# Kernel optimization log

Measured on AMD Instinct MI355X. Metric: run time of the kernel, lower is better.

The kernel has to match this reference:

```python
import jax, jax.numpy as jnp
import numpy as np

CLAMP_MIN = 1e-30
DIAG_SCALE = 10.0


def _fast_cdist(x1, x2):
    # mean-center both by x1's row-mean (as in torch source)
    adjustment = x1.mean(axis=-2, keepdims=True)
    x1 = x1 - adjustment
    x2 = x2 - adjustment
    x1_norm = jnp.sum(x1 * x1, axis=-1, keepdims=True)  # [N,1]
    x2_norm = jnp.sum(x2 * x2, axis=-1, keepdims=True)  # [N,1]
    # matmul trick: ||a-b||^2 = ||a||^2 + ||b||^2 - 2 a.b
    res = (-2.0) * (x1 @ x2.T) + x1_norm + x2_norm.T
    return jnp.sqrt(jnp.maximum(res, CLAMP_MIN))


def reference(x):
    # L2-normalize rows
    norm = jnp.linalg.norm(x, axis=-1, keepdims=True)
    x_norm = x / norm
    dist_mat = _fast_cdist(x_norm, x_norm)  # [N, N]
    d = jnp.diagonal(dist_mat)
    dist_mat = dist_mat + DIAG_SCALE * jnp.diag(1.0 - d)
    loss = jnp.max(1.0 / dist_mat, axis=1)
    return jnp.mean(loss)


def setup_inputs() -> dict:
    key = jax.random.key(0)
    x = jax.random.normal(key, (8192, 256), dtype=jnp.float32)
    return {"x": x}
```

## Files before the change

kernel.cpp:

```cpp
#include <hip/hip_runtime.h>
#include <stdint.h>

#define N_ROWS 8192
#define N_DIM  256
#define NB     64
#define NTRI   2080

typedef __attribute__((ext_vector_type(8))) short bf16x8;
typedef __attribute__((ext_vector_type(4))) float f32x4;

__device__ inline unsigned short f2bf(float f) {
    unsigned u = __float_as_uint(f);
    unsigned r = (u + 0x7FFFu + ((u >> 16) & 1u)) >> 16;
    return (unsigned short)r;
}
__device__ inline float bf2f(unsigned short b) {
    return __uint_as_float(((unsigned)b) << 16);
}
__device__ inline unsigned encf(float f) {
    unsigned u = __float_as_uint(f);
    return u ^ ((u & 0x80000000u) ? 0xFFFFFFFFu : 0x80000000u);
}
__device__ inline float decf(unsigned e) {
    unsigned u = e ^ ((e & 0x80000000u) ? 0x80000000u : 0xFFFFFFFFu);
    return __uint_as_float(u);
}
#define ENC_BIG 0xF149F2CAu


__global__ __launch_bounds__(256) void k_norm_fast(const float* __restrict__ x,
                                                   char* __restrict__ zf,
                                                   float* __restrict__ nsq,
                                                   unsigned* __restrict__ rmin,
                                                   float* __restrict__ out) {
    if (blockIdx.x == 0 && threadIdx.x == 0) *out = 0.0f;
    const int lane = threadIdx.x & 63;
    const int w    = threadIdx.x >> 6;
    const int row  = blockIdx.x * 4 + w;
    const float4* xr = (const float4*)(x + (size_t)row * N_DIM);
    float4 v = xr[lane];
    float ss = v.x*v.x + v.y*v.y + v.z*v.z + v.w*v.w;
    #pragma unroll
    for (int m = 1; m < 64; m <<= 1) ss += __shfl_xor(ss, m, 64);
    const float inv = 1.0f / sqrtf(ss);
    unsigned short b0 = f2bf(v.x * inv);
    unsigned short b1 = f2bf(v.y * inv);
    unsigned short b2 = f2bf(v.z * inv);
    unsigned short b3 = f2bf(v.w * inv);
    ushort4 uv; uv.x = b0; uv.y = b1; uv.z = b2; uv.w = b3;
    *(ushort4*)(zf + ((size_t)(row >> 4) << 13) + ((lane >> 1) << 8) +
                ((row & 15) << 4) + ((lane & 1) << 3)) = uv;
    float z0 = bf2f(b0), z1 = bf2f(b1), z2 = bf2f(b2), z3 = bf2f(b3);
    float s2 = z0*z0 + z1*z1 + z2*z2 + z3*z3;
    #pragma unroll
    for (int m = 1; m < 64; m <<= 1) s2 += __shfl_xor(s2, m, 64);
    if (lane == 0) {
        nsq[row]  = s2;
        rmin[row] = ENC_BIG;
    }
}

__global__ __launch_bounds__(256, 3) void k_gemm_fast(const char* __restrict__ zf,
                                                      const float* __restrict__ nsq,
                                                      unsigned* __restrict__ rmin) {
    __shared__ float pminR[128][2];
    __shared__ float pminC[128][2];

    const int tid   = threadIdx.x;
    const int lane  = tid & 63;
    const int w     = tid >> 6;
    const int waveM = (w >> 1) * 64;
    const int waveN = (w & 1) * 64;

    const int t = blockIdx.x;
    int br = (int)((129.0f - sqrtf(16641.0f - 8.0f * (float)t)) * 0.5f);
    while ((br + 1) * (129 - (br + 1)) / 2 <= t) ++br;
    while (br * (129 - br) / 2 > t) --br;
    const int bc = br + (t - br * (129 - br) / 2);
    const bool isdiag = (br == bc);

    const int aBlk = br * 8 + (waveM >> 4);
    const int bBlk = bc * 8 + (waveN >> 4);

    f32x4 acc[4][4];
    #pragma unroll
    for (int m = 0; m < 4; ++m)
        #pragma unroll
        for (int n = 0; n < 4; ++n)
            acc[m][n] = (f32x4){0.f, 0.f, 0.f, 0.f};

    const char* laneA = zf + (size_t)aBlk * 8192 + lane * 16;
    const char* laneB = zf + (size_t)bBlk * 8192 + lane * 16;

    #pragma unroll
    for (int s = 0; s < 8; ++s) {
        bf16x8 af[4], bfr[4];
        #pragma unroll
        for (int m = 0; m < 4; ++m)
            af[m] = *(const bf16x8*)(laneA + (size_t)m * 8192 + s * 1024);
        #pragma unroll
        for (int n = 0; n < 4; ++n)
            bfr[n] = *(const bf16x8*)(laneB + (size_t)n * 8192 + s * 1024);
        #pragma unroll
        for (int m = 0; m < 4; ++m)
            #pragma unroll
            for (int n = 0; n < 4; ++n)
                acc[m][n] = __builtin_amdgcn_mfma_f32_16x16x32_bf16(af[m], bfr[n], acc[m][n], 0, 0, 0);
    }

    asm volatile("" ::: "memory");

    float nj[4];
    #pragma unroll
    for (int n = 0; n < 4; ++n)
        nj[n] = nsq[bc * 128 + waveN + n * 16 + (lane & 15)];
    float4 ni4[4];
    #pragma unroll
    for (int m = 0; m < 4; ++m)
        ni4[m] = *(const float4*)&nsq[br * 128 + waveM + m * 16 + (lane >> 4) * 4];

    float rminv[4][4];
    float cminv[4];
    #pragma unroll
    for (int m = 0; m < 4; ++m)
        #pragma unroll
        for (int r = 0; r < 4; ++r)
            rminv[m][r] = 1e30f;
    #pragma unroll
    for (int n = 0; n < 4; ++n)
        cminv[n] = 1e30f;

    const int lrow0 = waveM + (lane >> 4) * 4;
    const int lcol0 = waveN + (lane & 15);
    #pragma unroll
    for (int m = 0; m < 4; ++m) {
        #pragma unroll
        for (int r = 0; r < 4; ++r) {
            const int lr = lrow0 + m * 16 + r;
            const float nir = ((const float*)&ni4[m])[r];
            #pragma unroll
            for (int n = 0; n < 4; ++n) {
                float u = fmaf(-2.0f, acc[m][n][r], nir + nj[n]);
                const bool diag = isdiag && (lr == (lcol0 + n * 16));
                u = diag ? 1e30f : u;
                rminv[m][r] = fminf(rminv[m][r], u);
                cminv[n]    = fminf(cminv[n], u);
            }
        }
    }
    #pragma unroll
    for (int mask = 1; mask < 16; mask <<= 1)
        #pragma unroll
        for (int m = 0; m < 4; ++m)
            #pragma unroll
            for (int r = 0; r < 4; ++r)
                rminv[m][r] = fminf(rminv[m][r], __shfl_xor(rminv[m][r], mask, 64));
    if ((lane & 15) == 0) {
        const int q = lane >> 4;
        #pragma unroll
        for (int m = 0; m < 4; ++m)
            #pragma unroll
            for (int r = 0; r < 4; ++r)
                pminR[waveM + m * 16 + q * 4 + r][w & 1] = rminv[m][r];
    }
    if (!isdiag) {
        #pragma unroll
        for (int mask = 16; mask < 64; mask <<= 1)
            #pragma unroll
            for (int n = 0; n < 4; ++n)
                cminv[n] = fminf(cminv[n], __shfl_xor(cminv[n], mask, 64));
        if (lane < 16) {
            #pragma unroll
            for (int n = 0; n < 4; ++n)
                pminC[waveN + n * 16 + lane][w >> 1] = cminv[n];
        }
    }
    __syncthreads();
    if (tid < 128) {
        const float v = fminf(pminR[tid][0], pminR[tid][1]);
        atomicMin(&rmin[br * 128 + tid], encf(v));
        if (!isdiag) {
            const float vc = fminf(pminC[tid][0], pminC[tid][1]);
            atomicMin(&rmin[bc * 128 + tid], encf(vc));
        }
    }
}

__global__ __launch_bounds__(256) void k_norm_fb(const float* x,
                                                 char* zb, long zstride,
                                                 char* nsqb, long nstride,
                                                 char* rminb, long rstride,
                                                 float* out) {
    if (blockIdx.x == 0 && threadIdx.x == 0) *out = 0.0f;
    const int lane = threadIdx.x & 63;
    const int w    = threadIdx.x >> 6;
    const int row  = blockIdx.x * 4 + w;
    const float4* xr = (const float4*)(x + (size_t)row * N_DIM);
    float4 v = xr[lane];
    float ss = v.x*v.x + v.y*v.y + v.z*v.z + v.w*v.w;
    #pragma unroll
    for (int m = 1; m < 64; m <<= 1) ss += __shfl_xor(ss, m, 64);
    const float inv = 1.0f / sqrtf(ss);
    unsigned short b0 = f2bf(v.x * inv), b1 = f2bf(v.y * inv);
    unsigned short b2 = f2bf(v.z * inv), b3 = f2bf(v.w * inv);
    ushort4 uv; uv.x = b0; uv.y = b1; uv.z = b2; uv.w = b3;
    *(ushort4*)(zb + (size_t)row * zstride + lane * 8) = uv;
    float z0 = bf2f(b0), z1 = bf2f(b1), z2 = bf2f(b2), z3 = bf2f(b3);
    float s2 = z0*z0 + z1*z1 + z2*z2 + z3*z3;
    #pragma unroll
    for (int m = 1; m < 64; m <<= 1) s2 += __shfl_xor(s2, m, 64);
    if (lane == 0) {
        *(float*)(nsqb + (size_t)row * nstride) = s2;
        *(unsigned*)(rminb + (size_t)row * rstride) = ENC_BIG;
    }
}

#define GLD_LDS16(g, l)                                                        \
    __builtin_amdgcn_global_load_lds(                                          \
        (const __attribute__((address_space(1))) unsigned int*)(g),            \
        (__attribute__((address_space(3))) unsigned int*)(l), 16, 0, 0)

__global__ __launch_bounds__(256, 4) void k_gemm_fb(const char* zb, long zstride,
                                                    const char* nsqb, long nstride,
                                                    char* rminb, long rstride) {
    __shared__ unsigned short As[128 * 64];
    __shared__ unsigned short Bs[128 * 64];
    __shared__ float pminR[128][2];
    __shared__ float pminC[128][2];

    const int tid   = threadIdx.x;
    const int lane  = tid & 63;
    const int w     = tid >> 6;
    const int waveM = (w >> 1) * 64;
    const int waveN = (w & 1) * 64;

    const int t = blockIdx.x;
    int br = (int)((129.0f - sqrtf(16641.0f - 8.0f * (float)t)) * 0.5f);
    while ((br + 1) * (129 - (br + 1)) / 2 <= t) ++br;
    while (br * (129 - br) / 2 > t) --br;
    const int bc = br + (t - br * (129 - br) / 2);
    const bool isdiag = (br == bc);

    const char* gA = zb + (size_t)br * 128 * zstride;
    const char* gB = zb + (size_t)bc * 128 * zstride;

    f32x4 acc[4][4];
    #pragma unroll
    for (int m = 0; m < 4; ++m)
        #pragma unroll
        for (int n = 0; n < 4; ++n)
            acc[m][n] = (f32x4){0.f, 0.f, 0.f, 0.f};

    for (int kk = 0; kk < 4; ++kk) {
        __syncthreads();
        #pragma unroll
        for (int c = 0; c < 4; ++c) {
            const int f    = c * 4096 + tid * 16;
            const int row  = f >> 7;
            const int slot = (f >> 4) & 7;
            const int c_g  = slot ^ (row & 7);
            GLD_LDS16(gA + (size_t)row * zstride + kk * 128 + c_g * 16,
                      (char*)As + c * 4096 + w * 1024);
            GLD_LDS16(gB + (size_t)row * zstride + kk * 128 + c_g * 16,
                      (char*)Bs + c * 4096 + w * 1024);
        }
        __syncthreads();

        #pragma unroll
        for (int s = 0; s < 2; ++s) {
            bf16x8 af[4], bfr[4];
            const int q = (lane >> 4) + s * 4;
            #pragma unroll
            for (int m = 0; m < 4; ++m) {
                const int rr = waveM + m * 16 + (lane & 15);
                af[m] = *(const bf16x8*)&As[rr * 64 + ((q ^ (rr & 7)) << 3)];
            }
            #pragma unroll
            for (int n = 0; n < 4; ++n) {
                const int rr = waveN + n * 16 + (lane & 15);
                bfr[n] = *(const bf16x8*)&Bs[rr * 64 + ((q ^ (rr & 7)) << 3)];
            }
            #pragma unroll
            for (int m = 0; m < 4; ++m)
                #pragma unroll
                for (int n = 0; n < 4; ++n)
                    acc[m][n] = __builtin_amdgcn_mfma_f32_16x16x32_bf16(af[m], bfr[n], acc[m][n], 0, 0, 0);
        }
    }

    asm volatile("" ::: "memory");

    float nj[4];
    #pragma unroll
    for (int n = 0; n < 4; ++n)
        nj[n] = *(const float*)(nsqb + (size_t)(bc * 128 + waveN + n * 16 + (lane & 15)) * nstride);
    float4 ni4[4];
    #pragma unroll
    for (int m = 0; m < 4; ++m) {
        const int row0 = br * 128 + waveM + m * 16 + (lane >> 4) * 4;
        ni4[m].x = *(const float*)(nsqb + (size_t)(row0 + 0) * nstride);
        ni4[m].y = *(const float*)(nsqb + (size_t)(row0 + 1) * nstride);
        ni4[m].z = *(const float*)(nsqb + (size_t)(row0 + 2) * nstride);
        ni4[m].w = *(const float*)(nsqb + (size_t)(row0 + 3) * nstride);
    }

    float rminv[4][4];
    float cminv[4];
    #pragma unroll
    for (int m = 0; m < 4; ++m)
        #pragma unroll
        for (int r = 0; r < 4; ++r)
            rminv[m][r] = 1e30f;
    #pragma unroll
    for (int n = 0; n < 4; ++n)
        cminv[n] = 1e30f;

    const int lrow0 = waveM + (lane >> 4) * 4;
    const int lcol0 = waveN + (lane & 15);
    #pragma unroll
    for (int m = 0; m < 4; ++m) {
        #pragma unroll
        for (int r = 0; r < 4; ++r) {
            const int lr = lrow0 + m * 16 + r;
            const float nir = ((const float*)&ni4[m])[r];
            #pragma unroll
            for (int n = 0; n < 4; ++n) {
                float u = fmaf(-2.0f, acc[m][n][r], nir + nj[n]);
                const bool diag = isdiag && (lr == (lcol0 + n * 16));
                u = diag ? 1e30f : u;
                rminv[m][r] = fminf(rminv[m][r], u);
                cminv[n]    = fminf(cminv[n], u);
            }
        }
    }
    #pragma unroll
    for (int mask = 1; mask < 16; mask <<= 1)
        #pragma unroll
        for (int m = 0; m < 4; ++m)
            #pragma unroll
            for (int r = 0; r < 4; ++r)
                rminv[m][r] = fminf(rminv[m][r], __shfl_xor(rminv[m][r], mask, 64));
    if ((lane & 15) == 0) {
        const int q = lane >> 4;
        #pragma unroll
        for (int m = 0; m < 4; ++m)
            #pragma unroll
            for (int r = 0; r < 4; ++r)
                pminR[waveM + m * 16 + q * 4 + r][w & 1] = rminv[m][r];
    }
    if (!isdiag) {
        #pragma unroll
        for (int mask = 16; mask < 64; mask <<= 1)
            #pragma unroll
            for (int n = 0; n < 4; ++n)
                cminv[n] = fminf(cminv[n], __shfl_xor(cminv[n], mask, 64));
        if (lane < 16) {
            #pragma unroll
            for (int n = 0; n < 4; ++n)
                pminC[waveN + n * 16 + lane][w >> 1] = cminv[n];
        }
    }
    __syncthreads();
    if (tid < 128) {
        const float v = fminf(pminR[tid][0], pminR[tid][1]);
        atomicMin((unsigned*)(rminb + (size_t)(br * 128 + tid) * rstride), encf(v));
        if (!isdiag) {
            const float vc = fminf(pminC[tid][0], pminC[tid][1]);
            atomicMin((unsigned*)(rminb + (size_t)(bc * 128 + tid) * rstride), encf(vc));
        }
    }
}

__global__ __launch_bounds__(256) void k_final(const char* nsqb, long nstride,
                                               const char* rminb, long rstride,
                                               float* out) {
    const int r = blockIdx.x * 256 + threadIdx.x;
    const float mn  = decf(*(const unsigned*)(rminb + (size_t)r * rstride));
    const float res = fmaxf(mn, 1e-30f);
    float loss = fmaxf(1.0f / sqrtf(res), 0.1f);
    #pragma unroll
    for (int m = 1; m < 64; m <<= 1) loss += __shfl_xor(loss, m, 64);
    __shared__ float wsum[4];
    const int lane = threadIdx.x & 63, w = threadIdx.x >> 6;
    if (lane == 0) wsum[w] = loss;
    __syncthreads();
    if (threadIdx.x == 0)
        atomicAdd(out, (wsum[0] + wsum[1] + wsum[2] + wsum[3]) * (1.0f / 8192.0f));
}

extern "C" void kernel_launch(void* const* d_in, const int* in_sizes, int n_in,
                              void* d_out, int out_size, void* d_ws, size_t ws_size,
                              hipStream_t stream) {
    float* x   = (float*)d_in[0];
    float* out = (float*)d_out;
    char*  ws  = (char*)d_ws;

    const size_t WS_NEED = 4u * 1024 * 1024 + 64 * 1024 + 4096;
    if (ws_size >= WS_NEED) {
        char*     zf   = ws;
        float*    nsq  = (float*)(ws + 4u * 1024 * 1024);
        unsigned* rmin = (unsigned*)(ws + 4u * 1024 * 1024 + 32 * 1024);
        k_norm_fast<<<N_ROWS / 4, 256, 0, stream>>>(x, zf, nsq, rmin, out);
        k_gemm_fast<<<NTRI, 256, 0, stream>>>(zf, nsq, rmin);
        k_final<<<N_ROWS / 256, 256, 0, stream>>>((const char*)nsq, 4,
                                                  (const char*)rmin, 4, out);
    } else {
        char* zb    = (char*)x;       long zstride = 1024;
        char* nsqb  = (char*)x + 512; long nstride = 1024;
        char* rminb = (char*)x + 516; long rstride = 1024;
        k_norm_fb<<<N_ROWS / 4, 256, 0, stream>>>(x, zb, zstride, nsqb, nstride, rminb, rstride, out);
        k_gemm_fb<<<NTRI, 256, 0, stream>>>(zb, zstride, nsqb, nstride, rminb, rstride);
        k_final<<<N_ROWS / 256, 256, 0, stream>>>(nsqb, nstride, rminb, rstride, out);
    }
}
```

Measured before the change: 91.21 us.

## Stage shared A tile in LDS and triple-buffer B fragments in registers

The fast GEMM kernel used to have every wave load its A fragments straight from global memory, so the two waves sharing a row block fetched the same data twice. Now the block's 128-row A tile is loaded into 32KB of LDS in two halves with global_load_lds, and the waves read their fragments from there. B fragments are prefetched two k-steps ahead into a three-slot register ring to hide global latency. This adds LDS use and barriers, and the extra registers and shared memory may lower occupancy below the declared 3 blocks per CU.

```diff
diff --git a/kernel.cpp b/kernel.cpp
--- a/kernel.cpp
+++ b/kernel.cpp
@@ -26,6 +26,11 @@
     return __uint_as_float(u);
 }
 #define ENC_BIG 0xF149F2CAu
+
+#define GLD_LDS16(g, l)                                                        \
+    __builtin_amdgcn_global_load_lds(                                          \
+        (const __attribute__((address_space(1))) unsigned int*)(g),            \
+        (__attribute__((address_space(3))) unsigned int*)(l), 16, 0, 0)
 
 
 __global__ __launch_bounds__(256) void k_norm_fast(const float* __restrict__ x,
@@ -63,6 +68,7 @@
 __global__ __launch_bounds__(256, 3) void k_gemm_fast(const char* __restrict__ zf,
                                                       const float* __restrict__ nsq,
                                                       unsigned* __restrict__ rmin) {
+    __shared__ char  As[32 * 1024];
     __shared__ float pminR[128][2];
     __shared__ float pminC[128][2];
 
@@ -79,8 +85,8 @@
     const int bc = br + (t - br * (129 - br) / 2);
     const bool isdiag = (br == bc);
 
-    const int aBlk = br * 8 + (waveM >> 4);
-    const int bBlk = bc * 8 + (waveN >> 4);
+    const char* gA    = zf + (size_t)br * 65536;
+    const char* laneB = zf + ((size_t)(bc * 8 + (waveN >> 4))) * 8192 + lane * 16;
 
     f32x4 acc[4][4];
     #pragma unroll
@@ -89,23 +95,41 @@
         for (int n = 0; n < 4; ++n)
             acc[m][n] = (f32x4){0.f, 0.f, 0.f, 0.f};
 
-    const char* laneA = zf + (size_t)aBlk * 8192 + lane * 16;
-    const char* laneB = zf + (size_t)bBlk * 8192 + lane * 16;
-
-    #pragma unroll
-    for (int s = 0; s < 8; ++s) {
-        bf16x8 af[4], bfr[4];
-        #pragma unroll
-        for (int m = 0; m < 4; ++m)
-            af[m] = *(const bf16x8*)(laneA + (size_t)m * 8192 + s * 1024);
-        #pragma unroll
-        for (int n = 0; n < 4; ++n)
-            bfr[n] = *(const bf16x8*)(laneB + (size_t)n * 8192 + s * 1024);
-        #pragma unroll
-        for (int m = 0; m < 4; ++m)
-            #pragma unroll
-            for (int n = 0; n < 4; ++n)
-                acc[m][n] = __builtin_amdgcn_mfma_f32_16x16x32_bf16(af[m], bfr[n], acc[m][n], 0, 0, 0);
+    bf16x8 bbuf[3][4];
+    #pragma unroll
+    for (int n = 0; n < 4; ++n) bbuf[0][n] = *(const bf16x8*)(laneB + (size_t)n * 8192 + 0 * 1024);
+    #pragma unroll
+    for (int n = 0; n < 4; ++n) bbuf[1][n] = *(const bf16x8*)(laneB + (size_t)n * 8192 + 1 * 1024);
+
+    #pragma unroll
+    for (int h = 0; h < 2; ++h) {
+        __syncthreads();
+        #pragma unroll
+        for (int c = 0; c < 8; ++c)
+            GLD_LDS16(gA + (size_t)c * 8192 + h * 4096 + w * 1024 + lane * 16,
+                      As + c * 4096 + w * 1024);
+        __syncthreads();
+
+        #pragma unroll
+        for (int s = 0; s < 4; ++s) {
+            const int g = h * 4 + s;
+            if (g + 2 < 8) {
+                #pragma unroll
+                for (int n = 0; n < 4; ++n)
+                    bbuf[(g + 2) % 3][n] =
+                        *(const bf16x8*)(laneB + (size_t)n * 8192 + (g + 2) * 1024);
+            }
+            bf16x8 af[4];
+            #pragma unroll
+            for (int m = 0; m < 4; ++m)
+                af[m] = *(const bf16x8*)&As[((waveM >> 4) + m) * 4096 + s * 1024 + lane * 16];
+            #pragma unroll
+            for (int m = 0; m < 4; ++m)
+                #pragma unroll
+                for (int n = 0; n < 4; ++n)
+                    acc[m][n] = __builtin_amdgcn_mfma_f32_16x16x32_bf16(
+                        af[m], bbuf[g % 3][n], acc[m][n], 0, 0, 0);
+        }
     }
 
     asm volatile("" ::: "memory");
@@ -214,11 +238,6 @@
         *(unsigned*)(rminb + (size_t)row * rstride) = ENC_BIG;
     }
 }
-
-#define GLD_LDS16(g, l)                                                        \
-    __builtin_amdgcn_global_load_lds(                                          \
-        (const __attribute__((address_space(1))) unsigned int*)(g),            \
-        (__attribute__((address_space(3))) unsigned int*)(l), 16, 0, 0)
 
 __global__ __launch_bounds__(256, 4) void k_gemm_fb(const char* zb, long zstride,
                                                     const char* nsqb, long nstride,
```

Measured after the change: 88.94 us. 1.03x faster.

## Use 256x256 tiles with 16 waves and double-buffered LDS staging in Gram kernel

Applied to the files above, without the earlier changes.

Changes the fast Gram kernel from 128x128 upper-triangular tiles with 4 waves loading fragments straight from global memory to 256x256 tiles with 16 waves per 1024-thread block. Operand K-slices are staged into double-buffered shared memory with global_load_lds, so each wave's fragments are shared across waves rather than fetched repeatedly. This is meant to cut redundant global/L2 traffic and to overlap loads with MFMA work. In exchange there are far fewer blocks (528 vs 2080), which raises the risk of poor occupancy, tail imbalance across CUs, and extra barrier cost. The diagonal blocks also waste more work with the larger tiles.

```diff
diff --git a/kernel.cpp b/kernel.cpp
--- a/kernel.cpp
+++ b/kernel.cpp
@@ -5,6 +5,8 @@
 #define N_DIM  256
 #define NB     64
 #define NTRI   2080
+#define NB2    32
+#define NTRI2  528
 
 typedef __attribute__((ext_vector_type(8))) short bf16x8;
 typedef __attribute__((ext_vector_type(4))) float f32x4;
@@ -26,6 +28,11 @@
     return __uint_as_float(u);
 }
 #define ENC_BIG 0xF149F2CAu
+
+#define GLD_LDS16(g, l)                                                        \
+    __builtin_amdgcn_global_load_lds(                                          \
+        (const __attribute__((address_space(1))) unsigned int*)(g),            \
+        (__attribute__((address_space(3))) unsigned int*)(l), 16, 0, 0)
 
 
 __global__ __launch_bounds__(256) void k_norm_fast(const float* __restrict__ x,
@@ -60,27 +67,33 @@
     }
 }
 
-__global__ __launch_bounds__(256, 3) void k_gemm_fast(const char* __restrict__ zf,
-                                                      const float* __restrict__ nsq,
-                                                      unsigned* __restrict__ rmin) {
-    __shared__ float pminR[128][2];
-    __shared__ float pminC[128][2];
+__global__ __launch_bounds__(1024) void k_gemm_fast(const char* __restrict__ zf,
+                                                    const float* __restrict__ nsq,
+                                                    unsigned* __restrict__ rmin) {
+    __shared__ char S[65536];
 
     const int tid   = threadIdx.x;
     const int lane  = tid & 63;
     const int w     = tid >> 6;
-    const int waveM = (w >> 1) * 64;
-    const int waveN = (w & 1) * 64;
+    const int wm    = w >> 2;
+    const int wn    = w & 3;
+    const int waveM = wm * 64;
+    const int waveN = wn * 64;
 
     const int t = blockIdx.x;
-    int br = (int)((129.0f - sqrtf(16641.0f - 8.0f * (float)t)) * 0.5f);
-    while ((br + 1) * (129 - (br + 1)) / 2 <= t) ++br;
-    while (br * (129 - br) / 2 > t) --br;
-    const int bc = br + (t - br * (129 - br) / 2);
+    int br = (int)((65.0f - sqrtf(4225.0f - 8.0f * (float)t)) * 0.5f);
+    while ((br + 1) * (65 - (br + 1)) / 2 <= t) ++br;
+    while (br * (65 - br) / 2 > t) --br;
+    const int bc = br + (t - br * (65 - br) / 2);
     const bool isdiag = (br == bc);
 
-    const int aBlk = br * 8 + (waveM >> 4);
-    const int bBlk = bc * 8 + (waveN >> 4);
+#define STAGE(s, buf)                                                          \
+    do {                                                                       \
+        GLD_LDS16(zf + ((size_t)(br * 16 + w) << 13) + ((s) << 10) + lane * 16,\
+                  S + (buf) * 32768 + w * 1024);                               \
+        GLD_LDS16(zf + ((size_t)(bc * 16 + w) << 13) + ((s) << 10) + lane * 16,\
+                  S + (buf) * 32768 + 16384 + w * 1024);                       \
+    } while (0)
 
     f32x4 acc[4][4];
     #pragma unroll
@@ -89,35 +102,38 @@
         for (int n = 0; n < 4; ++n)
             acc[m][n] = (f32x4){0.f, 0.f, 0.f, 0.f};
 
-    const char* laneA = zf + (size_t)aBlk * 8192 + lane * 16;
-    const char* laneB = zf + (size_t)bBlk * 8192 + lane * 16;
-
+    STAGE(0, 0);
+    __syncthreads();
     #pragma unroll
     for (int s = 0; s < 8; ++s) {
+        const int buf = s & 1;
+        if (s < 7) STAGE(s + 1, buf ^ 1);
         bf16x8 af[4], bfr[4];
         #pragma unroll
         for (int m = 0; m < 4; ++m)
-            af[m] = *(const bf16x8*)(laneA + (size_t)m * 8192 + s * 1024);
+            af[m] = *(const bf16x8*)(S + buf * 32768 + (wm * 4 + m) * 1024 + lane * 16);
         #pragma unroll
         for (int n = 0; n < 4; ++n)
-            bfr[n] = *(const bf16x8*)(laneB + (size_t)n * 8192 + s * 1024);
+            bfr[n] = *(const bf16x8*)(S + buf * 32768 + 16384 + (wn * 4 + n) * 1024 + lane * 16);
         #pragma unroll
         for (int m = 0; m < 4; ++m)
             #pragma unroll
             for (int n = 0; n < 4; ++n)
                 acc[m][n] = __builtin_amdgcn_mfma_f32_16x16x32_bf16(af[m], bfr[n], acc[m][n], 0, 0, 0);
-    }
+        if (s < 7) __syncthreads();
+    }
+#undef STAGE
 
     asm volatile("" ::: "memory");
 
     float nj[4];
     #pragma unroll
     for (int n = 0; n < 4; ++n)
-        nj[n] = nsq[bc * 128 + waveN + n * 16 + (lane & 15)];
+        nj[n] = nsq[bc * 256 + waveN + n * 16 + (lane & 15)];
     float4 ni4[4];
     #pragma unroll
     for (int m = 0; m < 4; ++m)
-        ni4[m] = *(const float4*)&nsq[br * 128 + waveM + m * 16 + (lane >> 4) * 4];
+        ni4[m] = *(const float4*)&nsq[br * 256 + waveM + m * 16 + (lane >> 4) * 4];
 
     float rminv[4][4];
     float cminv[4];
@@ -155,13 +171,16 @@
             #pragma unroll
             for (int r = 0; r < 4; ++r)
                 rminv[m][r] = fminf(rminv[m][r], __shfl_xor(rminv[m][r], mask, 64));
+
+    float* pmR = (float*)S;
+    float* pmC = (float*)(S + 4096);
     if ((lane & 15) == 0) {
         const int q = lane >> 4;
         #pragma unroll
         for (int m = 0; m < 4; ++m)
             #pragma unroll
             for (int r = 0; r < 4; ++r)
-                pminR[waveM + m * 16 + q * 4 + r][w & 1] = rminv[m][r];
+                pmR[(waveM + m * 16 + q * 4 + r) * 4 + wn] = rminv[m][r];
     }
     if (!isdiag) {
         #pragma unroll
@@ -172,16 +191,18 @@
         if (lane < 16) {
             #pragma unroll
             for (int n = 0; n < 4; ++n)
-                pminC[waveN + n * 16 + lane][w >> 1] = cminv[n];
+                pmC[(waveN + n * 16 + lane) * 4 + wm] = cminv[n];
         }
     }
     __syncthreads();
-    if (tid < 128) {
-        const float v = fminf(pminR[tid][0], pminR[tid][1]);
-        atomicMin(&rmin[br * 128 + tid], encf(v));
+    if (tid < 256) {
+        const float v = fminf(fminf(pmR[tid * 4 + 0], pmR[tid * 4 + 1]),
+                              fminf(pmR[tid * 4 + 2], pmR[tid * 4 + 3]));
+        atomicMin(&rmin[br * 256 + tid], encf(v));
         if (!isdiag) {
-            const float vc = fminf(pminC[tid][0], pminC[tid][1]);
-            atomicMin(&rmin[bc * 128 + tid], encf(vc));
+            const float vc = fminf(fminf(pmC[tid * 4 + 0], pmC[tid * 4 + 1]),
+                                   fminf(pmC[tid * 4 + 2], pmC[tid * 4 + 3]));
+            atomicMin(&rmin[bc * 256 + tid], encf(vc));
         }
     }
 }
@@ -215,11 +236,6 @@
     }
 }
 
-#define GLD_LDS16(g, l)                                                        \
-    __builtin_amdgcn_global_load_lds(                                          \
-        (const __attribute__((address_space(1))) unsigned int*)(g),            \
-        (__attribute__((address_space(3))) unsigned int*)(l), 16, 0, 0)
-
 __global__ __launch_bounds__(256, 4) void k_gemm_fb(const char* zb, long zstride,
                                                     const char* nsqb, long nstride,
                                                     char* rminb, long rstride) {
@@ -401,7 +417,7 @@
         float*    nsq  = (float*)(ws + 4u * 1024 * 1024);
         unsigned* rmin = (unsigned*)(ws + 4u * 1024 * 1024 + 32 * 1024);
         k_norm_fast<<<N_ROWS / 4, 256, 0, stream>>>(x, zf, nsq, rmin, out);
-        k_gemm_fast<<<NTRI, 256, 0, stream>>>(zf, nsq, rmin);
+        k_gemm_fast<<<NTRI2, 1024, 0, stream>>>(zf, nsq, rmin);
         k_final<<<N_ROWS / 256, 256, 0, stream>>>((const char*)nsq, 4,
                                                   (const char*)rmin, 4, out);
     } else {
```

Measured after the change: 95.34 us. 4.5% more time.
